# Optimization experiments

Hardware: AMD Instinct MI355X
Metric: run time of the kernel (lower is better)

Reference implementation:

```python
import jax, jax.numpy as jnp
import numpy as np
import math

B, N, D, O, H = 8, 1024, 512, 512, 8
HD = O // H  # head_dim = 64


def setup_inputs() -> dict:
    key = jax.random.key(0)
    ks = jax.random.split(key, 12)
    x = jax.random.normal(ks[0], (B, N, D), dtype=jnp.float32)
    adj = jax.random.uniform(ks[1], (B, N, N), dtype=jnp.float32)  # unused by forward math
    mask = jax.random.randint(ks[2], (B, N), 0, 2) > 0  # bool padding mask
    # learned params (torch nn.Linear: y = x @ W.T + b)
    qkv_w = jax.random.normal(ks[3], (3 * O, D), dtype=jnp.float32) / math.sqrt(D)
    qkv_b = jnp.zeros((3 * O,), dtype=jnp.float32)
    # self_loop_W: 1/head_dim + U(0,1), per head, non-trainable
    self_loop_W = (1.0 / HD + jax.random.uniform(ks[4], (1, H, 1, 1))).astype(jnp.float32)
    w1 = jax.random.normal(ks[5], (O, O), dtype=jnp.float32) / math.sqrt(O)
    b1 = jnp.zeros((O,), dtype=jnp.float32)
    w2 = jax.random.normal(ks[6], (O, O), dtype=jnp.float32) / math.sqrt(O)
    b2 = jnp.zeros((O,), dtype=jnp.float32)
    wr = jax.random.normal(ks[7], (O, D), dtype=jnp.float32) / math.sqrt(D)
    br = jnp.zeros((O,), dtype=jnp.float32)
    return {"x": x, "adj": adj, "mask": mask, "self_loop_W": self_loop_W,
            "qkv_w": qkv_w, "qkv_b": qkv_b, "w1": w1, "b1": b1,
            "w2": w2, "b2": b2, "wr": wr, "br": br}


def reference(x, adj, mask, self_loop_W, qkv_w, qkv_b, w1, b1, w2, b2, wr, br):
    fmask = mask.astype(x.dtype)  # [B,N]
    # --- MoireAttention ---
    qkv = x @ qkv_w.T + qkv_b                       # [B,N,3O]
    qkv = qkv.reshape(B, N, 3, H, HD).transpose(2, 0, 3, 1, 4)  # [3,B,H,N,hd]
    Q, K, V = qkv[0], qkv[1], qkv[2]
    scores = jnp.einsum('bhnd,bhmd->bhnm', Q, K) / math.sqrt(HD)  # [B,H,N,N]
    eye = jnp.eye(N, dtype=scores.dtype)
    scores = scores + eye[None, None] * self_loop_W  # per-head diagonal self-loop bias
    mask2d = mask[:, None, :, None] & mask[:, None, None, :]  # [B,1,N,N]
    scores = jnp.where(mask2d, scores, jnp.asarray(-1e6, scores.dtype))
    attn = jax.nn.softmax(scores, axis=-1)
    h = jnp.einsum('bhnm,bhmd->bhnd', attn, V)      # [B,H,N,hd]
    h = h.transpose(0, 2, 1, 3).reshape(B, N, O)
    # --- mask, FFN (eval mode: noise/dropout are identity), mask ---
    h = h * fmask[..., None]
    h = jax.nn.relu(h @ w1.T + b1) @ w2.T + b2
    h = h * fmask[..., None]
    # --- residual blend ---
    x_proj = x @ wr.T + br
    return h * 0.5 + x_proj * 0.5
```

## Files before the change

### kernel.cpp

```cpp
#include <hip/hip_runtime.h>
#include <hip/hip_bf16.h>

typedef __attribute__((ext_vector_type(8))) short short8;
typedef __attribute__((ext_vector_type(4))) float f32x4;
typedef __attribute__((ext_vector_type(4))) short short4v;

#define BB 8
#define NN 1024
#define DD 512
#define OO 512
#define HH 8
#define HD 64
#define MM (BB * NN)

#define QSC 0.18033688f
#define KSHIFT -11.54156032f
#define KMASKED -30000.0f

__device__ __forceinline__ void gload_lds16(const void* g, void* l) {
  __builtin_amdgcn_global_load_lds(
      (const __attribute__((address_space(1))) void*)g,
      (__attribute__((address_space(3))) void*)l, 16, 0, 0);
}

__device__ __forceinline__ uint2 cvt4(float4 v) {
  union { uint2 u; __hip_bfloat16 h[4]; } t;
  t.h[0] = __float2bfloat16(v.x);
  t.h[1] = __float2bfloat16(v.y);
  t.h[2] = __float2bfloat16(v.z);
  t.h[3] = __float2bfloat16(v.w);
  return t.u;
}

#define SEG_N 10
struct ConvArgs {
  const float* src[SEG_N];
  __hip_bfloat16* dst[SEG_N];
  int n4[SEG_N];
};

__global__ void convert_kernel(ConvArgs a) {
  const int t = blockIdx.y;
  const int n4 = a.n4[t];
  const float4* fs = (const float4*)a.src[t];
  uint2* d = (uint2*)a.dst[t];
  for (int i = blockIdx.x * blockDim.x + threadIdx.x; i < n4;
       i += gridDim.x * blockDim.x)
    d[i] = cvt4(fs[i]);
}

__global__ __launch_bounds__(256) void gemm_qkv(
    const __hip_bfloat16* __restrict__ A0, const __hip_bfloat16* __restrict__ B0,
    const __hip_bfloat16* __restrict__ bias0,
    __hip_bfloat16* __restrict__ out0, __hip_bfloat16* __restrict__ out1,
    __hip_bfloat16* __restrict__ out2, int Kd) {
  __shared__ __align__(16) __hip_bfloat16 smem[8192];
  __hip_bfloat16* As = smem;
  __hip_bfloat16* Bs = smem + 4096;

  const int tid  = threadIdx.x;
  const int wave = tid >> 6;
  const int lane = tid & 63;
  const int fl   = lane & 15;
  const int fk   = (lane >> 4) * 8;
  const int wm   = (wave & 1) * 64;
  const int wn   = (wave >> 1) * 64;
  const int bid     = blockIdx.x;
  const int rowpart = 8 * (bid & 7) + ((bid >> 3) & 7);
  const int colpart = bid >> 6;
  const int m0 = rowpart * 128;
  const int n0 = colpart * 128;
  const int glr  = lane >> 2;
  const int glc  = (lane & 3) * 8;

  f32x4 acc[4][4];
#pragma unroll
  for (int i = 0; i < 4; ++i)
#pragma unroll
    for (int j = 0; j < 4; ++j) acc[i][j] = (f32x4){0.f, 0.f, 0.f, 0.f};

  char* lb = (char*)smem;
  for (int k0 = 0; k0 < Kd; k0 += 32) {
    __syncthreads();
    gload_lds16(A0 + (size_t)(m0 + wave * 16 + glr) * Kd + k0 + glc,
                lb + wave * 1024 + lane * 16);
    gload_lds16(A0 + (size_t)(m0 + 64 + wave * 16 + glr) * Kd + k0 + glc,
                lb + (wave + 4) * 1024 + lane * 16);
    gload_lds16(B0 + (size_t)(n0 + wave * 16 + glr) * Kd + k0 + glc,
                lb + 8192 + wave * 1024 + lane * 16);
    gload_lds16(B0 + (size_t)(n0 + 64 + wave * 16 + glr) * Kd + k0 + glc,
                lb + 8192 + (wave + 4) * 1024 + lane * 16);
    __syncthreads();

    short8 af[4], bfr[4];
#pragma unroll
    for (int i = 0; i < 4; ++i)
      af[i] = *(const short8*)&As[(wm + i * 16 + fl) * 32 + fk];
#pragma unroll
    for (int j = 0; j < 4; ++j)
      bfr[j] = *(const short8*)&Bs[(wn + j * 16 + fl) * 32 + fk];
#pragma unroll
    for (int i = 0; i < 4; ++i)
#pragma unroll
      for (int j = 0; j < 4; ++j)
        acc[i][j] = __builtin_amdgcn_mfma_f32_16x16x32_bf16(af[i], bfr[j],
                                                            acc[i][j], 0, 0, 0);
  }

  const int rb = (lane >> 4) * 4;
  const int part = n0 >> 9;
  if (part < 2) {
    __hip_bfloat16* dst = (part == 0) ? out0 : out1;
    const float scf = (part == 0) ? QSC : 1.0f;
#pragma unroll
    for (int j = 0; j < 4; ++j) {
      const int colb  = n0 + wn + j * 16;
      const int o     = colb & 511;
      const int headq = o >> 6;
      const int d     = (o & 63) + fl;
      const float bi  = __bfloat162float(bias0[colb + fl]);
#pragma unroll
      for (int i = 0; i < 4; ++i) {
#pragma unroll
        for (int r = 0; r < 4; ++r) {
          const int row = m0 + wm + i * 16 + rb + r;
          const int bb  = row >> 10;
          const int nn  = row & 1023;
          dst[((size_t)((bb << 3) + headq) * NN + nn) * HD + d] =
              __float2bfloat16((acc[i][j][r] + bi) * scf);
        }
      }
    }
  } else {
    __syncthreads();
    __hip_bfloat16* tsc = smem + wave * 1120;
    const int bb  = (m0 + wm) >> 10;
    const int nnb = (m0 + wm) & 1023;
    const int dl  = lane >> 2;
    const int cc  = (lane & 3) * 16;
#pragma unroll
    for (int j = 0; j < 4; ++j) {
      const int colb  = n0 + wn + j * 16;
      const int o     = colb & 511;
      const int headq = o >> 6;
      const int dbase = o & 63;
      const float bi  = __bfloat162float(bias0[colb + fl]);
#pragma unroll
      for (int i = 0; i < 4; ++i) {
#pragma unroll
        for (int r = 0; r < 4; ++r) {
          const int rr = i * 16 + rb + r;
          tsc[fl * 70 + rr] = __float2bfloat16(acc[i][j][r] + bi);
        }
      }
      uint4 r0 = *(const uint4*)&tsc[dl * 70 + cc];
      uint4 r1 = *(const uint4*)&tsc[dl * 70 + cc + 8];
      __hip_bfloat16* vdst =
          out2 + ((size_t)((bb << 3) + headq) * HD + dbase + dl) * NN + nnb;
      *(uint4*)&vdst[cc] = r0;
      *(uint4*)&vdst[cc + 8] = r1;
    }
  }
}

__global__ __launch_bounds__(512) void ffn_fused(
    const __hip_bfloat16* __restrict__ hb, const __hip_bfloat16* __restrict__ xc,
    const __hip_bfloat16* __restrict__ w1, const __hip_bfloat16* __restrict__ w2,
    const __hip_bfloat16* __restrict__ wr,
    const __hip_bfloat16* __restrict__ b1, const __hip_bfloat16* __restrict__ b2,
    const __hip_bfloat16* __restrict__ br,
    const int* __restrict__ mask, float* __restrict__ outf) {
  __shared__ __align__(16) __hip_bfloat16 h1s[32 * 520];
  __shared__ __align__(16) __hip_bfloat16 xs[32 * 520];
  __shared__ float Mrow[32];

  const int tid  = threadIdx.x;
  const int wv   = tid >> 6;
  const int lane = tid & 63;
  const int fl   = lane & 15;
  const int quad = lane >> 4;
  const int fk   = quad * 8;
  const int m0   = blockIdx.x * 32;

  {
    const int col = (tid & 63) * 8;
#pragma unroll
    for (int c = 0; c < 4; ++c) {
      const int row = c * 8 + (tid >> 6);
      *(uint4*)&h1s[row * 520 + col] =
          *(const uint4*)&hb[(size_t)(m0 + row) * OO + col];
      *(uint4*)&xs[row * 520 + col] =
          *(const uint4*)&xc[(size_t)(m0 + row) * DD + col];
    }
    if (tid < 32) Mrow[tid] = (mask[m0 + tid] != 0) ? 1.f : 0.f;
  }
  __syncthreads();

  f32x4 acc[2][4];

  auto run_phase = [&](const __hip_bfloat16* __restrict__ W,
                       const __hip_bfloat16* __restrict__ Bsrc) {
    const __hip_bfloat16* wl0 = W + (size_t)(wv * 64 + fl) * 512 + fk;
    short8 a0[4], a1[4];
#pragma unroll
    for (int j = 0; j < 4; ++j) a0[j] = *(const short8*)(wl0 + j * 8192);
    for (int k = 0; k < 16; k += 2) {
#pragma unroll
      for (int j = 0; j < 4; ++j)
        a1[j] = *(const short8*)(wl0 + (k + 1) * 32 + j * 8192);
#pragma unroll
      for (int i = 0; i < 2; ++i) {
        const short8 bh = *(const short8*)&Bsrc[(i * 16 + fl) * 520 + k * 32 + fk];
#pragma unroll
        for (int j = 0; j < 4; ++j)
          acc[i][j] = __builtin_amdgcn_mfma_f32_16x16x32_bf16(a0[j], bh,
                                                              acc[i][j], 0, 0, 0);
      }
      if (k + 2 < 16) {
#pragma unroll
        for (int j = 0; j < 4; ++j)
          a0[j] = *(const short8*)(wl0 + (k + 2) * 32 + j * 8192);
      }
#pragma unroll
      for (int i = 0; i < 2; ++i) {
        const short8 bh =
            *(const short8*)&Bsrc[(i * 16 + fl) * 520 + k * 32 + 32 + fk];
#pragma unroll
        for (int j = 0; j < 4; ++j)
          acc[i][j] = __builtin_amdgcn_mfma_f32_16x16x32_bf16(a1[j], bh,
                                                              acc[i][j], 0, 0, 0);
      }
    }
  };

  const float mr0 = Mrow[fl];
  const float mr1 = Mrow[16 + fl];

#pragma unroll
  for (int i = 0; i < 2; ++i)
#pragma unroll
    for (int j = 0; j < 4; ++j) acc[i][j] = (f32x4){0.f, 0.f, 0.f, 0.f};
  run_phase(w1, h1s);
  __syncthreads();

#pragma unroll
  for (int j = 0; j < 4; ++j) {
    const int c0 = wv * 64 + j * 16 + quad * 4;
    union { short4v s; __hip_bfloat16 h[4]; } bv;
    bv.s = *(const short4v*)&b1[c0];
#pragma unroll
    for (int i = 0; i < 2; ++i) {
      const float mr = (i == 0) ? mr0 : mr1;
      union { short4v s; __hip_bfloat16 h[4]; } pu;
#pragma unroll
      for (int e = 0; e < 4; ++e) {
        const float v = fmaxf(acc[i][j][e] + __bfloat162float(bv.h[e]), 0.f) * mr;
        pu.h[e] = __float2bfloat16(v);
      }
      *(short4v*)&h1s[(i * 16 + fl) * 520 + c0] = pu.s;
    }
  }
  __syncthreads();

#pragma unroll
  for (int i = 0; i < 2; ++i)
#pragma unroll
    for (int j = 0; j < 4; ++j) acc[i][j] = (f32x4){0.f, 0.f, 0.f, 0.f};
  run_phase(w2, h1s);
  run_phase(wr, xs);

#pragma unroll
  for (int j = 0; j < 4; ++j) {
    const int c0 = wv * 64 + j * 16 + quad * 4;
    union { short4v s; __hip_bfloat16 h[4]; } b2v, brv;
    b2v.s = *(const short4v*)&b2[c0];
    brv.s = *(const short4v*)&br[c0];
#pragma unroll
    for (int i = 0; i < 2; ++i) {
      const float mr = (i == 0) ? mr0 : mr1;
      const int row = m0 + i * 16 + fl;
      float4 o;
      o.x = 0.5f * (acc[i][j][0] + __bfloat162float(brv.h[0]) +
                    mr * __bfloat162float(b2v.h[0]));
      o.y = 0.5f * (acc[i][j][1] + __bfloat162float(brv.h[1]) +
                    mr * __bfloat162float(b2v.h[1]));
      o.z = 0.5f * (acc[i][j][2] + __bfloat162float(brv.h[2]) +
                    mr * __bfloat162float(b2v.h[2]));
      o.w = 0.5f * (acc[i][j][3] + __bfloat162float(brv.h[3]) +
                    mr * __bfloat162float(b2v.h[3]));
      *(float4*)&outf[(size_t)row * OO + c0] = o;
    }
  }
}

__global__ __launch_bounds__(512) void attn_kernel(
    const __hip_bfloat16* __restrict__ Qb, const __hip_bfloat16* __restrict__ Kb,
    const __hip_bfloat16* __restrict__ Vt, const __hip_bfloat16* __restrict__ slw,
    const int* __restrict__ mask, __hip_bfloat16* __restrict__ hb) {
  __shared__ __align__(16) __hip_bfloat16 QPs[128 * 72];
  __shared__ __align__(16) __hip_bfloat16 Ks[64 * 72];
  __shared__ __align__(16) __hip_bfloat16 Vs[64 * 72];
  __shared__ float Msf[NN];

  const int tid  = threadIdx.x;
  const int wave = tid >> 6;
  const int lane = tid & 63;
  const int fl   = lane & 15;
  const int quad = lane >> 4;
  const int fk   = quad * 8;
  const int rb   = quad * 4;
  const int bh   = blockIdx.x & 63;
  const int qblk = blockIdx.x >> 6;
  const int b    = bh >> 3;
  const int head = bh & 7;
  const int q0   = qblk * 128;

  const float slwL2 = __bfloat162float(slw[head]) * 1.44269504f;

  {
    const int srow = tid >> 2;
    const int sc   = (tid & 3) * 16;
    const __hip_bfloat16* qg = Qb + ((size_t)bh * NN + q0) * HD;
    uint4 v0 = *(const uint4*)(qg + srow * HD + sc);
    uint4 v1 = *(const uint4*)(qg + srow * HD + sc + 8);
    *(uint4*)&QPs[srow * 72 + sc] = v0;
    *(uint4*)&QPs[srow * 72 + sc + 8] = v1;
#pragma unroll
    for (int k = 0; k < 2; ++k) {
      const int idx = tid * 2 + k;
      Msf[idx] = (mask[b * NN + idx] != 0) ? KSHIFT : KMASKED;
    }
  }
  __syncthreads();
  const short8 qa0 = *(const short8*)&QPs[(wave * 16 + fl) * 72 + fk];
  const short8 qa1 = *(const short8*)&QPs[(wave * 16 + fl) * 72 + fk + 32];

  const int srow2 = tid >> 3;
  const int sc2   = (tid & 7) * 8;

  const __hip_bfloat16* kgb = Kb + (size_t)bh * NN * HD;
  const __hip_bfloat16* vgb = Vt + (size_t)bh * HD * NN;

  uint4 kr = *(const uint4*)(kgb + (size_t)srow2 * HD + sc2);
  uint4 vr = *(const uint4*)(vgb + (size_t)srow2 * NN + sc2);

  float lsum = 0.f;
  f32x4 Oacc[4];
#pragma unroll
  for (int t = 0; t < 4; ++t) Oacc[t] = (f32x4){0.f, 0.f, 0.f, 0.f};

  const int kbdiag = 2 * qblk + (wave >> 2);

  for (int kb = 0; kb < NN / 64; ++kb) {
    const int kbase = kb * 64;
    __syncthreads();
    *(uint4*)&Ks[srow2 * 72 + sc2] = kr;
    *(uint4*)&Vs[srow2 * 72 + sc2] = vr;
    __syncthreads();

    if (kb + 1 < NN / 64) {
      const int nk = kbase + 64;
      kr = *(const uint4*)(kgb + (size_t)(nk + srow2) * HD + sc2);
      vr = *(const uint4*)(vgb + (size_t)srow2 * NN + nk + sc2);
    }

    f32x4 sfr[4];
    __builtin_amdgcn_s_setprio(1);
#pragma unroll
    for (int j = 0; j < 4; ++j) {
      const short8 kf0 = *(const short8*)&Ks[(j * 16 + fl) * 72 + fk];
      const short8 kf1 = *(const short8*)&Ks[(j * 16 + fl) * 72 + fk + 32];
      f32x4 z = (f32x4){0.f, 0.f, 0.f, 0.f};
      z = __builtin_amdgcn_mfma_f32_16x16x32_bf16(kf0, qa0, z, 0, 0, 0);
      z = __builtin_amdgcn_mfma_f32_16x16x32_bf16(kf1, qa1, z, 0, 0, 0);
      sfr[j] = z;
    }
    __builtin_amdgcn_s_setprio(0);

    if (kb == kbdiag) {
      if ((fl >> 2) == quad) sfr[wave & 3][fl & 3] += slwL2;
    }

#pragma unroll
    for (int j = 0; j < 4; ++j) {
      const f32x4 mb4 = *(const f32x4*)&Msf[kbase + j * 16 + quad * 4];
      union { short4v s; __hip_bfloat16 h[4]; } pu;
      float ps = 0.f;
#pragma unroll
      for (int e = 0; e < 4; ++e) {
        const float pv = exp2f(sfr[j][e] + mb4[e]);
        ps += pv;
        pu.h[e] = __float2bfloat16(pv);
      }
      lsum += ps;
      *(short4v*)&QPs[(wave * 16 + fl) * 72 + j * 16 + quad * 4] = pu.s;
    }

    const short8 pa0 = *(const short8*)&QPs[(wave * 16 + fl) * 72 + fk];
    const short8 pa1 = *(const short8*)&QPs[(wave * 16 + fl) * 72 + fk + 32];
    __builtin_amdgcn_s_setprio(1);
#pragma unroll
    for (int t = 0; t < 4; ++t) {
      const short8 vf0 = *(const short8*)&Vs[(t * 16 + fl) * 72 + fk];
      const short8 vf1 = *(const short8*)&Vs[(t * 16 + fl) * 72 + fk + 32];
      Oacc[t] = __builtin_amdgcn_mfma_f32_16x16x32_bf16(pa0, vf0, Oacc[t], 0, 0, 0);
      Oacc[t] = __builtin_amdgcn_mfma_f32_16x16x32_bf16(pa1, vf1, Oacc[t], 0, 0, 0);
    }
    __builtin_amdgcn_s_setprio(0);
  }

  float l = lsum;
  l += __shfl_xor(l, 16, 64);
  l += __shfl_xor(l, 32, 64);
  const int qrow_me = q0 + wave * 16 + fl;
  const float qm = (mask[b * NN + qrow_me] != 0) ? 1.f : 0.f;
  const float sf = qm / fmaxf(l, 1e-30f);

  float scl[4];
#pragma unroll
  for (int r = 0; r < 4; ++r) scl[r] = __shfl(sf, rb + r, 64);

#pragma unroll
  for (int t = 0; t < 4; ++t) {
    const int d = t * 16 + fl;
#pragma unroll
    for (int r = 0; r < 4; ++r) {
      const int qrow_g = q0 + wave * 16 + rb + r;
      hb[(size_t)(b * NN + qrow_g) * OO + head * HD + d] =
          __float2bfloat16(Oacc[t][r] * scl[r]);
    }
  }
}

extern "C" void kernel_launch(void* const* d_in, const int* in_sizes, int n_in,
                              void* d_out, int out_size, void* d_ws, size_t ws_size,
                              hipStream_t stream) {
  const float* x_raw    = (const float*)d_in[0];
  const int* mask       = (const int*)d_in[2];
  const float* slw_raw  = (const float*)d_in[3];
  const float* qkvw_raw = (const float*)d_in[4];
  const float* qkvb_raw = (const float*)d_in[5];
  const float* w1_raw   = (const float*)d_in[6];
  const float* b1_raw   = (const float*)d_in[7];
  const float* w2_raw   = (const float*)d_in[8];
  const float* b2_raw   = (const float*)d_in[9];
  const float* wr_raw   = (const float*)d_in[10];
  const float* br_raw   = (const float*)d_in[11];
  float* outf           = (float*)d_out;

  __hip_bfloat16* p = (__hip_bfloat16*)d_ws;
  __hip_bfloat16* xc    = p; p += (size_t)MM * DD;
  __hip_bfloat16* qkvwc = p; p += 3 * OO * DD;
  __hip_bfloat16* w1c   = p; p += OO * OO;
  __hip_bfloat16* w2c   = p; p += OO * OO;
  __hip_bfloat16* wrc   = p; p += OO * DD;
  __hip_bfloat16* qkvbc = p; p += 3 * OO;
  __hip_bfloat16* b1c   = p; p += OO;
  __hip_bfloat16* b2c   = p; p += OO;
  __hip_bfloat16* brc   = p; p += OO;
  __hip_bfloat16* slwc  = p; p += 64;
  const size_t ebuf = (size_t)BB * HH * NN * HD;
  __hip_bfloat16* Qb = p; p += ebuf;
  __hip_bfloat16* Kb = p; p += ebuf;
  __hip_bfloat16* Vb = p; p += ebuf;
  __hip_bfloat16* hb = (__hip_bfloat16*)d_out;

  if (ws_size < (size_t)((char*)p - (char*)d_ws)) return;

  ConvArgs ca;
  ca.src[0] = x_raw;    ca.dst[0] = xc;    ca.n4[0] = MM * DD / 4;
  ca.src[1] = qkvw_raw; ca.dst[1] = qkvwc; ca.n4[1] = 3 * OO * DD / 4;
  ca.src[2] = w1_raw;   ca.dst[2] = w1c;   ca.n4[2] = OO * OO / 4;
  ca.src[3] = w2_raw;   ca.dst[3] = w2c;   ca.n4[3] = OO * OO / 4;
  ca.src[4] = wr_raw;   ca.dst[4] = wrc;   ca.n4[4] = OO * DD / 4;
  ca.src[5] = qkvb_raw; ca.dst[5] = qkvbc; ca.n4[5] = 3 * OO / 4;
  ca.src[6] = b1_raw;   ca.dst[6] = b1c;   ca.n4[6] = OO / 4;
  ca.src[7] = b2_raw;   ca.dst[7] = b2c;   ca.n4[7] = OO / 4;
  ca.src[8] = br_raw;   ca.dst[8] = brc;   ca.n4[8] = OO / 4;
  ca.src[9] = slw_raw;  ca.dst[9] = slwc;  ca.n4[9] = HH / 4;
  convert_kernel<<<dim3(1024, SEG_N), 256, 0, stream>>>(ca);

  gemm_qkv<<<768, 256, 0, stream>>>(xc, qkvwc, qkvbc, Qb, Kb, Vb, DD);
  attn_kernel<<<BB * HH * (NN / 128), 512, 0, stream>>>(Qb, Kb, Vb, slwc, mask, hb);
  ffn_fused<<<256, 512, 0, stream>>>(hb, xc, w1c, w2c, wrc, b1c, b2c, brc,
                                     mask, outf);
}
```

Measured before the change: 222.2 us.

## Template FFN row block, use 16-row tiles with separate workspace buffer

The FFN kernel is templated on rows per block. When the workspace is large enough, the attention output goes into a separate workspace buffer instead of aliasing the output, and the FFN launches 512 blocks of 16 rows instead of 256 blocks of 32, which puts more blocks on the CUs. The weight-fragment prefetch now keeps four k-steps of A in registers with a fully unrolled k loop and raises wave priority with s_setprio around the MFMA groups. Halving the row tile doubles how often the weights are reloaded per output row, and the deeper prefetch adds register pressure.

```diff
diff --git a/kernel.cpp b/kernel.cpp
--- a/kernel.cpp
+++ b/kernel.cpp
@@ -163,6 +163,7 @@
   }
 }
 
+template <int RB>
 __global__ __launch_bounds__(512) void ffn_fused(
     const __hip_bfloat16* __restrict__ hb, const __hip_bfloat16* __restrict__ xc,
     const __hip_bfloat16* __restrict__ w1, const __hip_bfloat16* __restrict__ w2,
@@ -170,9 +171,10 @@
     const __hip_bfloat16* __restrict__ b1, const __hip_bfloat16* __restrict__ b2,
     const __hip_bfloat16* __restrict__ br,
     const int* __restrict__ mask, float* __restrict__ outf) {
-  __shared__ __align__(16) __hip_bfloat16 h1s[32 * 520];
-  __shared__ __align__(16) __hip_bfloat16 xs[32 * 520];
-  __shared__ float Mrow[32];
+  constexpr int R = RB / 16;
+  __shared__ __align__(16) __hip_bfloat16 h1s[RB * 520];
+  __shared__ __align__(16) __hip_bfloat16 xs[RB * 520];
+  __shared__ float Mrow[RB];
 
   const int tid  = threadIdx.x;
   const int wv   = tid >> 6;
@@ -180,64 +182,57 @@
   const int fl   = lane & 15;
   const int quad = lane >> 4;
   const int fk   = quad * 8;
-  const int m0   = blockIdx.x * 32;
+  const int m0   = blockIdx.x * RB;
 
   {
     const int col = (tid & 63) * 8;
 #pragma unroll
-    for (int c = 0; c < 4; ++c) {
+    for (int c = 0; c < RB / 8; ++c) {
       const int row = c * 8 + (tid >> 6);
       *(uint4*)&h1s[row * 520 + col] =
           *(const uint4*)&hb[(size_t)(m0 + row) * OO + col];
       *(uint4*)&xs[row * 520 + col] =
           *(const uint4*)&xc[(size_t)(m0 + row) * DD + col];
     }
-    if (tid < 32) Mrow[tid] = (mask[m0 + tid] != 0) ? 1.f : 0.f;
+    if (tid < RB) Mrow[tid] = (mask[m0 + tid] != 0) ? 1.f : 0.f;
   }
   __syncthreads();
 
-  f32x4 acc[2][4];
+  f32x4 acc[R][4];
 
   auto run_phase = [&](const __hip_bfloat16* __restrict__ W,
                        const __hip_bfloat16* __restrict__ Bsrc) {
     const __hip_bfloat16* wl0 = W + (size_t)(wv * 64 + fl) * 512 + fk;
-    short8 a0[4], a1[4];
-#pragma unroll
-    for (int j = 0; j < 4; ++j) a0[j] = *(const short8*)(wl0 + j * 8192);
-    for (int k = 0; k < 16; k += 2) {
+    short8 a[4][4];
+#pragma unroll
+    for (int d = 0; d < 4; ++d)
 #pragma unroll
       for (int j = 0; j < 4; ++j)
-        a1[j] = *(const short8*)(wl0 + (k + 1) * 32 + j * 8192);
-#pragma unroll
-      for (int i = 0; i < 2; ++i) {
-        const short8 bh = *(const short8*)&Bsrc[(i * 16 + fl) * 520 + k * 32 + fk];
+        a[d][j] = *(const short8*)(wl0 + d * 32 + j * 8192);
+#pragma unroll
+    for (int k = 0; k < 16; ++k) {
+      short8 bh[R];
+#pragma unroll
+      for (int i = 0; i < R; ++i)
+        bh[i] = *(const short8*)&Bsrc[(i * 16 + fl) * 520 + k * 32 + fk];
+      __builtin_amdgcn_s_setprio(1);
+#pragma unroll
+      for (int j = 0; j < 4; ++j)
+#pragma unroll
+        for (int i = 0; i < R; ++i)
+          acc[i][j] = __builtin_amdgcn_mfma_f32_16x16x32_bf16(a[k & 3][j], bh[i],
+                                                              acc[i][j], 0, 0, 0);
+      __builtin_amdgcn_s_setprio(0);
+      if (k < 12) {
 #pragma unroll
         for (int j = 0; j < 4; ++j)
-          acc[i][j] = __builtin_amdgcn_mfma_f32_16x16x32_bf16(a0[j], bh,
-                                                              acc[i][j], 0, 0, 0);
+          a[k & 3][j] = *(const short8*)(wl0 + (k + 4) * 32 + j * 8192);
       }
-      if (k + 2 < 16) {
-#pragma unroll
-        for (int j = 0; j < 4; ++j)
-          a0[j] = *(const short8*)(wl0 + (k + 2) * 32 + j * 8192);
-      }
-#pragma unroll
-      for (int i = 0; i < 2; ++i) {
-        const short8 bh =
-            *(const short8*)&Bsrc[(i * 16 + fl) * 520 + k * 32 + 32 + fk];
-#pragma unroll
-        for (int j = 0; j < 4; ++j)
-          acc[i][j] = __builtin_amdgcn_mfma_f32_16x16x32_bf16(a1[j], bh,
-                                                              acc[i][j], 0, 0, 0);
-      }
     }
   };
 
-  const float mr0 = Mrow[fl];
-  const float mr1 = Mrow[16 + fl];
-
-#pragma unroll
-  for (int i = 0; i < 2; ++i)
+#pragma unroll
+  for (int i = 0; i < R; ++i)
 #pragma unroll
     for (int j = 0; j < 4; ++j) acc[i][j] = (f32x4){0.f, 0.f, 0.f, 0.f};
   run_phase(w1, h1s);
@@ -249,8 +244,8 @@
     union { short4v s; __hip_bfloat16 h[4]; } bv;
     bv.s = *(const short4v*)&b1[c0];
 #pragma unroll
-    for (int i = 0; i < 2; ++i) {
-      const float mr = (i == 0) ? mr0 : mr1;
+    for (int i = 0; i < R; ++i) {
+      const float mr = Mrow[i * 16 + fl];
       union { short4v s; __hip_bfloat16 h[4]; } pu;
 #pragma unroll
       for (int e = 0; e < 4; ++e) {
@@ -263,7 +258,7 @@
   __syncthreads();
 
 #pragma unroll
-  for (int i = 0; i < 2; ++i)
+  for (int i = 0; i < R; ++i)
 #pragma unroll
     for (int j = 0; j < 4; ++j) acc[i][j] = (f32x4){0.f, 0.f, 0.f, 0.f};
   run_phase(w2, h1s);
@@ -276,8 +271,8 @@
     b2v.s = *(const short4v*)&b2[c0];
     brv.s = *(const short4v*)&br[c0];
 #pragma unroll
-    for (int i = 0; i < 2; ++i) {
-      const float mr = (i == 0) ? mr0 : mr1;
+    for (int i = 0; i < R; ++i) {
+      const float mr = Mrow[i * 16 + fl];
       const int row = m0 + i * 16 + fl;
       float4 o;
       o.x = 0.5f * (acc[i][j][0] + __bfloat162float(brv.h[0]) +
@@ -463,9 +458,12 @@
   __hip_bfloat16* Qb = p; p += ebuf;
   __hip_bfloat16* Kb = p; p += ebuf;
   __hip_bfloat16* Vb = p; p += ebuf;
-  __hip_bfloat16* hb = (__hip_bfloat16*)d_out;
-
-  if (ws_size < (size_t)((char*)p - (char*)d_ws)) return;
+
+  const size_t base_need = (size_t)((char*)p - (char*)d_ws);
+  if (ws_size < base_need) return;
+
+  const bool hb_ws = ws_size >= base_need + ebuf * sizeof(__hip_bfloat16);
+  __hip_bfloat16* hb = hb_ws ? p : (__hip_bfloat16*)d_out;
 
   ConvArgs ca;
   ca.src[0] = x_raw;    ca.dst[0] = xc;    ca.n4[0] = MM * DD / 4;
@@ -482,6 +480,10 @@
 
   gemm_qkv<<<768, 256, 0, stream>>>(xc, qkvwc, qkvbc, Qb, Kb, Vb, DD);
   attn_kernel<<<BB * HH * (NN / 128), 512, 0, stream>>>(Qb, Kb, Vb, slwc, mask, hb);
-  ffn_fused<<<256, 512, 0, stream>>>(hb, xc, w1c, w2c, wrc, b1c, b2c, brc,
-                                     mask, outf);
-}
+  if (hb_ws)
+    ffn_fused<16><<<512, 512, 0, stream>>>(hb, xc, w1c, w2c, wrc, b1c, b2c, brc,
+                                           mask, outf);
+  else
+    ffn_fused<32><<<256, 512, 0, stream>>>(hb, xc, w1c, w2c, wrc, b1c, b2c, brc,
+                                           mask, outf);
+}
```

Measured after the change: 263.5 us. 1.19x slower.

## Move residual projection into QKV GEMM and stage FFN weights through LDS

Applied to the files above, without the earlier changes.

The residual projection x@wr is now computed as a fourth column part of the QKV GEMM, which grows from 768 to 1024 blocks. It writes 0.5*(x_proj+br) straight into the output buffer, and the FFN kernel reads that back and adds its own result. The FFN kernel no longer streams weights from global memory into registers per wave. It loads 32-wide K slices cooperatively into an LDS buffer with two barriers per slice, which drops the x tile and the third GEMM phase. The attention buffer moves from the output buffer to workspace, and a scheduling barrier is added in the attention loop. The trade-offs are more barriers in the FFN, an extra fp32 read-modify-write of the output, and a larger QKV launch.

```diff
diff --git a/kernel.cpp b/kernel.cpp
--- a/kernel.cpp
+++ b/kernel.cpp
@@ -51,9 +51,9 @@
 
 __global__ __launch_bounds__(256) void gemm_qkv(
     const __hip_bfloat16* __restrict__ A0, const __hip_bfloat16* __restrict__ B0,
-    const __hip_bfloat16* __restrict__ bias0,
+    const __hip_bfloat16* __restrict__ bias0, const __hip_bfloat16* __restrict__ bias1,
     __hip_bfloat16* __restrict__ out0, __hip_bfloat16* __restrict__ out1,
-    __hip_bfloat16* __restrict__ out2, int Kd) {
+    __hip_bfloat16* __restrict__ out2, float* __restrict__ outf, int Kd) {
   __shared__ __align__(16) __hip_bfloat16 smem[8192];
   __hip_bfloat16* As = smem;
   __hip_bfloat16* Bs = smem + 4096;
@@ -131,7 +131,7 @@
         }
       }
     }
-  } else {
+  } else if (part == 2) {
     __syncthreads();
     __hip_bfloat16* tsc = smem + wave * 1120;
     const int bb  = (m0 + wm) >> 10;
@@ -160,18 +160,31 @@
       *(uint4*)&vdst[cc] = r0;
       *(uint4*)&vdst[cc + 8] = r1;
     }
+  } else {
+#pragma unroll
+    for (int j = 0; j < 4; ++j) {
+      const int colb = n0 + wn + j * 16;
+      const int o    = colb & 511;
+      const float bi = 0.5f * __bfloat162float(bias1[o + fl]);
+#pragma unroll
+      for (int i = 0; i < 4; ++i) {
+#pragma unroll
+        for (int r = 0; r < 4; ++r) {
+          const int row = m0 + wm + i * 16 + rb + r;
+          outf[(size_t)row * OO + o + fl] = 0.5f * acc[i][j][r] + bi;
+        }
+      }
+    }
   }
 }
 
 __global__ __launch_bounds__(512) void ffn_fused(
-    const __hip_bfloat16* __restrict__ hb, const __hip_bfloat16* __restrict__ xc,
+    const __hip_bfloat16* __restrict__ hb,
     const __hip_bfloat16* __restrict__ w1, const __hip_bfloat16* __restrict__ w2,
-    const __hip_bfloat16* __restrict__ wr,
     const __hip_bfloat16* __restrict__ b1, const __hip_bfloat16* __restrict__ b2,
-    const __hip_bfloat16* __restrict__ br,
     const int* __restrict__ mask, float* __restrict__ outf) {
   __shared__ __align__(16) __hip_bfloat16 h1s[32 * 520];
-  __shared__ __align__(16) __hip_bfloat16 xs[32 * 520];
+  __shared__ __align__(16) __hip_bfloat16 Ws[512 * 40];
   __shared__ float Mrow[32];
 
   const int tid  = threadIdx.x;
@@ -181,6 +194,8 @@
   const int quad = lane >> 4;
   const int fk   = quad * 8;
   const int m0   = blockIdx.x * 32;
+  const int tr   = tid >> 2;
+  const int tc8  = (tid & 3) * 8;
 
   {
     const int col = (tid & 63) * 8;
@@ -189,8 +204,6 @@
       const int row = c * 8 + (tid >> 6);
       *(uint4*)&h1s[row * 520 + col] =
           *(const uint4*)&hb[(size_t)(m0 + row) * OO + col];
-      *(uint4*)&xs[row * 520 + col] =
-          *(const uint4*)&xc[(size_t)(m0 + row) * DD + col];
     }
     if (tid < 32) Mrow[tid] = (mask[m0 + tid] != 0) ? 1.f : 0.f;
   }
@@ -198,49 +211,48 @@
 
   f32x4 acc[2][4];
 
-  auto run_phase = [&](const __hip_bfloat16* __restrict__ W,
-                       const __hip_bfloat16* __restrict__ Bsrc) {
-    const __hip_bfloat16* wl0 = W + (size_t)(wv * 64 + fl) * 512 + fk;
-    short8 a0[4], a1[4];
-#pragma unroll
-    for (int j = 0; j < 4; ++j) a0[j] = *(const short8*)(wl0 + j * 8192);
-    for (int k = 0; k < 16; k += 2) {
+  auto run_phase = [&](const __hip_bfloat16* __restrict__ W) {
+    uint4 wpre[4];
+#pragma unroll
+    for (int c = 0; c < 4; ++c)
+      wpre[c] = *(const uint4*)(W + (size_t)(c * 128 + tr) * 512 + tc8);
+    for (int k = 0; k < 16; ++k) {
+      __syncthreads();
+#pragma unroll
+      for (int c = 0; c < 4; ++c)
+        *(uint4*)&Ws[(c * 128 + tr) * 40 + tc8] = wpre[c];
+      __syncthreads();
+      if (k < 15) {
+#pragma unroll
+        for (int c = 0; c < 4; ++c)
+          wpre[c] = *(const uint4*)(W + (size_t)(c * 128 + tr) * 512 +
+                                    (k + 1) * 32 + tc8);
+      }
+      __builtin_amdgcn_sched_barrier(0);
+
+      short8 a_[4], bh_[2];
 #pragma unroll
       for (int j = 0; j < 4; ++j)
-        a1[j] = *(const short8*)(wl0 + (k + 1) * 32 + j * 8192);
-#pragma unroll
-      for (int i = 0; i < 2; ++i) {
-        const short8 bh = *(const short8*)&Bsrc[(i * 16 + fl) * 520 + k * 32 + fk];
-#pragma unroll
-        for (int j = 0; j < 4; ++j)
-          acc[i][j] = __builtin_amdgcn_mfma_f32_16x16x32_bf16(a0[j], bh,
+        a_[j] = *(const short8*)&Ws[(wv * 64 + j * 16 + fl) * 40 + fk];
+#pragma unroll
+      for (int i = 0; i < 2; ++i)
+        bh_[i] = *(const short8*)&h1s[(i * 16 + fl) * 520 + k * 32 + fk];
+      __builtin_amdgcn_s_setprio(1);
+#pragma unroll
+      for (int j = 0; j < 4; ++j)
+#pragma unroll
+        for (int i = 0; i < 2; ++i)
+          acc[i][j] = __builtin_amdgcn_mfma_f32_16x16x32_bf16(a_[j], bh_[i],
                                                               acc[i][j], 0, 0, 0);
-      }
-      if (k + 2 < 16) {
-#pragma unroll
-        for (int j = 0; j < 4; ++j)
-          a0[j] = *(const short8*)(wl0 + (k + 2) * 32 + j * 8192);
-      }
-#pragma unroll
-      for (int i = 0; i < 2; ++i) {
-        const short8 bh =
-            *(const short8*)&Bsrc[(i * 16 + fl) * 520 + k * 32 + 32 + fk];
-#pragma unroll
-        for (int j = 0; j < 4; ++j)
-          acc[i][j] = __builtin_amdgcn_mfma_f32_16x16x32_bf16(a1[j], bh,
-                                                              acc[i][j], 0, 0, 0);
-      }
+      __builtin_amdgcn_s_setprio(0);
     }
   };
 
-  const float mr0 = Mrow[fl];
-  const float mr1 = Mrow[16 + fl];
-
 #pragma unroll
   for (int i = 0; i < 2; ++i)
 #pragma unroll
     for (int j = 0; j < 4; ++j) acc[i][j] = (f32x4){0.f, 0.f, 0.f, 0.f};
-  run_phase(w1, h1s);
+  run_phase(w1);
   __syncthreads();
 
 #pragma unroll
@@ -250,7 +262,7 @@
     bv.s = *(const short4v*)&b1[c0];
 #pragma unroll
     for (int i = 0; i < 2; ++i) {
-      const float mr = (i == 0) ? mr0 : mr1;
+      const float mr = Mrow[i * 16 + fl];
       union { short4v s; __hip_bfloat16 h[4]; } pu;
 #pragma unroll
       for (int e = 0; e < 4; ++e) {
@@ -266,28 +278,23 @@
   for (int i = 0; i < 2; ++i)
 #pragma unroll
     for (int j = 0; j < 4; ++j) acc[i][j] = (f32x4){0.f, 0.f, 0.f, 0.f};
-  run_phase(w2, h1s);
-  run_phase(wr, xs);
+  run_phase(w2);
 
 #pragma unroll
   for (int j = 0; j < 4; ++j) {
     const int c0 = wv * 64 + j * 16 + quad * 4;
-    union { short4v s; __hip_bfloat16 h[4]; } b2v, brv;
+    union { short4v s; __hip_bfloat16 h[4]; } b2v;
     b2v.s = *(const short4v*)&b2[c0];
-    brv.s = *(const short4v*)&br[c0];
 #pragma unroll
     for (int i = 0; i < 2; ++i) {
-      const float mr = (i == 0) ? mr0 : mr1;
+      const float mr = Mrow[i * 16 + fl];
       const int row = m0 + i * 16 + fl;
+      float4 prev = *(const float4*)&outf[(size_t)row * OO + c0];
       float4 o;
-      o.x = 0.5f * (acc[i][j][0] + __bfloat162float(brv.h[0]) +
-                    mr * __bfloat162float(b2v.h[0]));
-      o.y = 0.5f * (acc[i][j][1] + __bfloat162float(brv.h[1]) +
-                    mr * __bfloat162float(b2v.h[1]));
-      o.z = 0.5f * (acc[i][j][2] + __bfloat162float(brv.h[2]) +
-                    mr * __bfloat162float(b2v.h[2]));
-      o.w = 0.5f * (acc[i][j][3] + __bfloat162float(brv.h[3]) +
-                    mr * __bfloat162float(b2v.h[3]));
+      o.x = prev.x + 0.5f * (acc[i][j][0] + mr * __bfloat162float(b2v.h[0]));
+      o.y = prev.y + 0.5f * (acc[i][j][1] + mr * __bfloat162float(b2v.h[1]));
+      o.z = prev.z + 0.5f * (acc[i][j][2] + mr * __bfloat162float(b2v.h[2]));
+      o.w = prev.w + 0.5f * (acc[i][j][3] + mr * __bfloat162float(b2v.h[3]));
       *(float4*)&outf[(size_t)row * OO + c0] = o;
     }
   }
@@ -363,6 +370,7 @@
       kr = *(const uint4*)(kgb + (size_t)(nk + srow2) * HD + sc2);
       vr = *(const uint4*)(vgb + (size_t)srow2 * NN + nk + sc2);
     }
+    __builtin_amdgcn_sched_barrier(0);
 
     f32x4 sfr[4];
     __builtin_amdgcn_s_setprio(1);
@@ -451,9 +459,9 @@
   __hip_bfloat16* p = (__hip_bfloat16*)d_ws;
   __hip_bfloat16* xc    = p; p += (size_t)MM * DD;
   __hip_bfloat16* qkvwc = p; p += 3 * OO * DD;
+  __hip_bfloat16* wrc   = p; p += OO * DD;
   __hip_bfloat16* w1c   = p; p += OO * OO;
   __hip_bfloat16* w2c   = p; p += OO * OO;
-  __hip_bfloat16* wrc   = p; p += OO * DD;
   __hip_bfloat16* qkvbc = p; p += 3 * OO;
   __hip_bfloat16* b1c   = p; p += OO;
   __hip_bfloat16* b2c   = p; p += OO;
@@ -463,7 +471,7 @@
   __hip_bfloat16* Qb = p; p += ebuf;
   __hip_bfloat16* Kb = p; p += ebuf;
   __hip_bfloat16* Vb = p; p += ebuf;
-  __hip_bfloat16* hb = (__hip_bfloat16*)d_out;
+  __hip_bfloat16* hb = p; p += ebuf;
 
   if (ws_size < (size_t)((char*)p - (char*)d_ws)) return;
 
@@ -480,8 +488,7 @@
   ca.src[9] = slw_raw;  ca.dst[9] = slwc;  ca.n4[9] = HH / 4;
   convert_kernel<<<dim3(1024, SEG_N), 256, 0, stream>>>(ca);
 
-  gemm_qkv<<<768, 256, 0, stream>>>(xc, qkvwc, qkvbc, Qb, Kb, Vb, DD);
+  gemm_qkv<<<1024, 256, 0, stream>>>(xc, qkvwc, qkvbc, brc, Qb, Kb, Vb, outf, DD);
   attn_kernel<<<BB * HH * (NN / 128), 512, 0, stream>>>(Qb, Kb, Vb, slwc, mask, hb);
-  ffn_fused<<<256, 512, 0, stream>>>(hb, xc, w1c, w2c, wrc, b1c, b2c, brc,
-                                     mask, outf);
-}
+  ffn_fused<<<256, 512, 0, stream>>>(hb, w1c, w2c, b1c, b2c, mask, outf);
+}
```

New measurement: 262.8 us. 1.18x slower.
